# Optimization experiments

Measured on AMD Instinct MI355X. Metric: run time of the kernel, lower is better.

## Reference

```python
import jax, jax.numpy as jnp
import numpy as np

D_MODEL = 2048
HQ = 32          # query heads
HKV = 8          # kv heads
HD = D_MODEL // HQ   # head_dim = 64
G = HQ // HKV        # group size = 4
THETA = 10000.0


def _rope(x, pos):
    """x: (B, H, T, D), pos: (B, T) int. Rotates even/odd interleaved pairs."""
    D = x.shape[-1]
    inv_freq = THETA ** (-jnp.arange(0, D, 2, dtype=jnp.float32) / D)   # (D/2,)
    ang = pos[:, None, :, None].astype(jnp.float32) * inv_freq          # (B,1,T,D/2)
    cos, sin = jnp.cos(ang), jnp.sin(ang)
    x1, x2 = x[..., 0::2], x[..., 1::2]
    r1 = x1 * cos - x2 * sin
    r2 = x1 * sin + x2 * cos
    return jnp.stack([r1, r2], axis=-1).reshape(x.shape)


def setup_inputs() -> dict:
    key = jax.random.key(0)
    ks = jax.random.split(key, 5)
    B, T = 2, 2048
    s = lambda fan_in: 1.0 / np.sqrt(fan_in)
    return {
        "x": jax.random.normal(ks[0], (B, T, D_MODEL), jnp.float32),
        "token_positions": jnp.arange(T, dtype=jnp.int32),
        "WQ": jax.random.normal(ks[1], (HQ * HD, D_MODEL), jnp.float32) * s(D_MODEL),
        "WK": jax.random.normal(ks[2], (HKV * HD, D_MODEL), jnp.float32) * s(D_MODEL),
        "WV": jax.random.normal(ks[3], (HKV * HD, D_MODEL), jnp.float32) * s(D_MODEL),
        "WO": jax.random.normal(ks[4], (D_MODEL, HQ * HD), jnp.float32) * s(HQ * HD),
    }


def reference(x, token_positions, WQ, WK, WV, WO):
    B, T, _ = x.shape
    pos = token_positions if token_positions.ndim == 2 else jnp.broadcast_to(token_positions[None, :], (B, T))

    # Projections (Linear is y = x @ W.T, no bias)
    Q = (x @ WQ.T).reshape(B, T, HQ, HD).transpose(0, 2, 1, 3)    # (B,Hq,T,D)
    K = (x @ WK.T).reshape(B, T, HKV, HD).transpose(0, 2, 1, 3)   # (B,Hkv,T,D)
    V = (x @ WV.T).reshape(B, T, HKV, HD).transpose(0, 2, 1, 3)

    Q = _rope(Q, pos)
    K = _rope(K, pos)

    # GQA: group query heads per kv head instead of duplicating K/V
    Qg = Q.reshape(B, HKV, G, T, HD)
    scale = jnp.float32(1.0 / np.sqrt(HD))
    scores = jnp.einsum('bkgqd,bkld->bkgql', Qg, K) * scale       # (B,Hkv,G,T,T)

    causal = jnp.tril(jnp.ones((T, T), dtype=bool))
    scores = jnp.where(causal, scores, jnp.finfo(scores.dtype).min)
    A = jax.nn.softmax(scores, axis=-1)

    O = jnp.einsum('bkgql,bkld->bkgqd', A, V)                     # (B,Hkv,G,T,D)
    O = O.reshape(B, HQ, T, HD).transpose(0, 2, 1, 3).reshape(B, T, HQ * HD)
    return O @ WO.T
```

## Files before the change

kernel.cpp:

```cpp
#include <hip/hip_runtime.h>
#include <hip/hip_bf16.h>

#define B_   2
#define T_   2048
#define DM_  2048
#define HQ_  32
#define HKV_ 8
#define HD_  64

typedef __attribute__((ext_vector_type(8))) short bf16x8;
typedef __attribute__((ext_vector_type(4))) float f32x4;
typedef __fp16 f16x4 __attribute__((ext_vector_type(4)));
typedef __fp16 f16x2 __attribute__((ext_vector_type(2)));

__device__ __forceinline__ unsigned short f2bf(float f) {
    unsigned int u = __float_as_uint(f);
    u = (u + 0x7fffu + ((u >> 16) & 1u)) >> 16;
    return (unsigned short)u;
}

__device__ __forceinline__ void gload16(const unsigned short* g, unsigned short* l) {
    __builtin_amdgcn_global_load_lds(
        (const __attribute__((address_space(1))) unsigned int*)g,
        (__attribute__((address_space(3))) unsigned int*)l, 16, 0, 0);
}


__global__ __launch_bounds__(256) void convert_all(
    const float* __restrict__ x,  const float* __restrict__ WQ,
    const float* __restrict__ WK, const float* __restrict__ WV,
    const float* __restrict__ WO, unsigned short* __restrict__ ws)
{
    int i = blockIdx.x*256 + threadIdx.x;
    const float* src; unsigned short* dst; int rel;
    if (i < 2097152)      { src = x;  dst = ws;                 rel = i; }
    else if (i < 3145728) { src = WQ; dst = ws + 8388608;       rel = i - 2097152; }
    else if (i < 3407872) { src = WK; dst = ws + 8388608+4194304; rel = i - 3145728; }
    else if (i < 3670016) { src = WV; dst = ws + 8388608+5242880; rel = i - 3407872; }
    else                  { src = WO; dst = ws + 14680064;      rel = i - 3670016; }
    float4 v = *(const float4*)(src + (size_t)rel*4);
    uint2 pk;
    pk.x = (unsigned int)f2bf(v.x) | ((unsigned int)f2bf(v.y) << 16);
    pk.y = (unsigned int)f2bf(v.z) | ((unsigned int)f2bf(v.w) << 16);
    *(uint2*)(dst + (size_t)rel*4) = pk;
}

__global__ __launch_bounds__(256) void qkv_gemm_bf16(
    const unsigned short* __restrict__ Ab, const unsigned short* __restrict__ Wb,
    unsigned short* __restrict__ Qb, unsigned short* __restrict__ Kb,
    unsigned short* __restrict__ Vt)
{
    __shared__ unsigned short As[128*32];
    __shared__ unsigned short Bs[128*32];
    const int tid  = threadIdx.x;
    const int ln   = tid & 63;
    const int wv   = tid >> 6;
    const int wm   = (wv >> 1) * 64;
    const int wn   = (wv & 1) * 64;
    const int col  = ln & 15;
    const int quad = ln >> 4;
    const int m0   = blockIdx.y * 128;
    const int n0   = blockIdx.x * 128;

    const unsigned short* aG = Ab + (size_t)(m0 + (tid>>2))*DM_ + (tid&3)*8;
    const unsigned short* bG = Wb + (size_t)(n0 + (tid>>2))*DM_ + (tid&3)*8;
    unsigned short* aL0 = &As[wv*512];
    unsigned short* aL1 = &As[wv*512 + 2048];
    unsigned short* bL0 = &Bs[wv*512];
    unsigned short* bL1 = &Bs[wv*512 + 2048];

    f32x4 acc[4][4];
    #pragma unroll
    for (int i=0;i<4;++i)
        #pragma unroll
        for (int j=0;j<4;++j) { acc[i][j][0]=0.f; acc[i][j][1]=0.f; acc[i][j][2]=0.f; acc[i][j][3]=0.f; }

    for (int k0 = 0; k0 < DM_; k0 += 32) {
        __syncthreads();
        gload16(aG + k0,                  aL0);
        gload16(aG + (size_t)64*DM_ + k0, aL1);
        gload16(bG + k0,                  bL0);
        gload16(bG + (size_t)64*DM_ + k0, bL1);
        __syncthreads();
        bf16x8 af[4], bfr[4];
        #pragma unroll
        for (int i=0;i<4;++i) {
            af[i]  = *(const bf16x8*)&As[(wm + i*16 + col)*32 + quad*8];
            bfr[i] = *(const bf16x8*)&Bs[(wn + i*16 + col)*32 + quad*8];
        }
        #pragma unroll
        for (int i=0;i<4;++i)
            #pragma unroll
            for (int j=0;j<4;++j)
                acc[i][j] = __builtin_amdgcn_mfma_f32_16x16x32_bf16(af[i], bfr[j], acc[i][j], 0, 0, 0);
    }

    const int b  = m0 >> 11;
    const int tb = m0 & 2047;
    #pragma unroll
    for (int j=0;j<4;++j) {
        const int n = n0 + wn + j*16 + col;
        #pragma unroll
        for (int i=0;i<4;++i) {
            const int t = tb + wm + i*16 + quad*4;
            if (n < 2048) {
                #pragma unroll
                for (int r=0;r<4;++r)
                    Qb[(((size_t)(b*HQ_ + (n>>6)))*T_ + t + r)*HD_ + (n&63)] = f2bf(acc[i][j][r]);
            } else if (n < 2560) {
                #pragma unroll
                for (int r=0;r<4;++r)
                    Kb[(((size_t)(b*HKV_ + ((n-2048)>>6)))*T_ + t + r)*HD_ + (n&63)] = f2bf(acc[i][j][r]);
            } else {
                unsigned short* vp = Vt + (((size_t)(b*HKV_ + ((n-2560)>>6)))*HD_ + (n&63))*T_ + t;
                union { f16x2 h; unsigned int u; } c0, c1;
                c0.h = __builtin_amdgcn_cvt_pkrtz(acc[i][j][0], acc[i][j][1]);
                c1.h = __builtin_amdgcn_cvt_pkrtz(acc[i][j][2], acc[i][j][3]);
                *(unsigned int*)(vp)     = c0.u;
                *(unsigned int*)(vp + 2) = c1.u;
            }
        }
    }
}

__global__ __launch_bounds__(256) void rope_inplace(
    unsigned short* __restrict__ Qb, unsigned short* __restrict__ Kb,
    const int* __restrict__ pos)
{
    const int NQ = B_*HQ_*T_*(HD_/2);
    const int NK = B_*HKV_*T_*(HD_/2);
    int idx = blockIdx.x*256 + threadIdx.x;
    unsigned short* base; float scale;
    int rem;
    if (idx < NQ) { base = Qb; rem = idx; scale = 0.18033688011112042f; }
    else { rem = idx - NQ; if (rem >= NK) return; base = Kb; scale = 1.0f; }
    const int i  = rem & 31;
    const int t  = (rem >> 5) & (T_ - 1);
    const int bh = rem >> 16;
    size_t off = (((size_t)bh)*T_ + t)*HD_ + (i<<1);
    unsigned int pk = *(unsigned int*)(base + off);
    float x1 = __uint_as_float((pk & 0xffffu) << 16);
    float x2 = __uint_as_float(pk & 0xffff0000u);
    float p = (float)pos[t];
    float inv = exp2f(-13.287712379549449f * ((float)(i<<1)) * (1.0f/64.0f));
    float ang = p * inv;
    float sn, cs;
    sincosf(ang, &sn, &cs);
    float r1 = (x1*cs - x2*sn) * scale;
    float r2 = (x1*sn + x2*cs) * scale;
    unsigned int out = (unsigned int)f2bf(r1) | ((unsigned int)f2bf(r2) << 16);
    *(unsigned int*)(base + off) = out;
}

__global__ __launch_bounds__(256, 2) void attn_mfma(
    const unsigned short* __restrict__ Qb, const unsigned short* __restrict__ Kb,
    const unsigned short* __restrict__ Vh, unsigned short* __restrict__ Ob)
{
    __shared__ unsigned short Ks[64*64];
    __shared__ unsigned short Vs[64*64];

    const int tid  = threadIdx.x;
    const int lane = tid & 63;
    const int wave = tid >> 6;
    const int q16  = lane & 15;
    const int quad = lane >> 4;
    const int bxi  = blockIdx.x;
    const int bh   = blockIdx.y;
    const int b    = bh >> 5;
    const int h    = bh & 31;
    const int kvh  = h >> 2;
    const int qa   = bxi;
    const int qbt  = 31 - bxi;
    const int qgA  = qa *64 + wave*16 + q16;
    const int qgB  = qbt*64 + wave*16 + q16;

    const unsigned short* kbase = Kb + ((size_t)(b*HKV_ + kvh))*T_*HD_;
    const unsigned short* vbase = Vh + ((size_t)(b*HKV_ + kvh))*(size_t)HD_*T_;

    const bf16x8 qA0 = *(const bf16x8*)(Qb + ((size_t)bh*T_ + qgA)*HD_ + quad*8);
    const bf16x8 qA1 = *(const bf16x8*)(Qb + ((size_t)bh*T_ + qgA)*HD_ + 32 + quad*8);
    const bf16x8 qB0 = *(const bf16x8*)(Qb + ((size_t)bh*T_ + qgB)*HD_ + quad*8);
    const bf16x8 qB1 = *(const bf16x8*)(Qb + ((size_t)bh*T_ + qgB)*HD_ + 32 + quad*8);

    f32x4 oA[4], oB[4];
    #pragma unroll
    for (int i=0;i<4;++i) {
        oA[i][0]=0.f; oA[i][1]=0.f; oA[i][2]=0.f; oA[i][3]=0.f;
        oB[i][0]=0.f; oB[i][1]=0.f; oB[i][2]=0.f; oB[i][3]=0.f;
    }
    float lA = 0.f, lB = 0.f;

    const int sr = tid >> 3;
    const int sj = tid & 7;
    const int sc = (sj ^ (sr & 7)) * 8;
    uint4 kr0, kr1, vr0, vr1;

    const int rk7 = q16 & 7;
    const int ck0 = (quad ^ rk7) * 8;
    const int ck1 = ((quad + 4) ^ rk7) * 8;

    kr0 = *(const uint4*)(kbase + (size_t)sr*HD_ + sj*8);
    kr1 = *(const uint4*)(kbase + (size_t)(sr+32)*HD_ + sj*8);
    vr0 = *(const uint4*)(vbase + (size_t)sr*T_ + sj*8);
    vr1 = *(const uint4*)(vbase + (size_t)(sr+32)*T_ + sj*8);

    for (int kt = 0; kt <= qbt; ++kt) {
        const int k0 = kt * 64;
        __syncthreads();
        *(uint4*)&Ks[sr*64 + sc]      = kr0;
        *(uint4*)&Ks[(sr+32)*64 + sc] = kr1;
        *(uint4*)&Vs[sr*64 + sc]      = vr0;
        *(uint4*)&Vs[(sr+32)*64 + sc] = vr1;
        __syncthreads();
        if (kt < qbt) {
            const int kn = k0 + 64;
            kr0 = *(const uint4*)(kbase + (size_t)(kn+sr)*HD_ + sj*8);
            kr1 = *(const uint4*)(kbase + (size_t)(kn+sr+32)*HD_ + sj*8);
            vr0 = *(const uint4*)(vbase + (size_t)sr*T_ + kn + sj*8);
            vr1 = *(const uint4*)(vbase + (size_t)(sr+32)*T_ + kn + sj*8);
        }
        const bool doA = (kt <= qa);

        f32x4 sAq[4], sBq[4];
        #pragma unroll
        for (int t=0;t<4;++t) {
            sAq[t][0]=0.f; sAq[t][1]=0.f; sAq[t][2]=0.f; sAq[t][3]=0.f;
            sBq[t][0]=0.f; sBq[t][1]=0.f; sBq[t][2]=0.f; sBq[t][3]=0.f;
        }
        #pragma unroll
        for (int t = 0; t < 4; ++t) {
            const int rk = (t*16 + q16) * 64;
            bf16x8 a0 = *(const bf16x8*)&Ks[rk + ck0];
            bf16x8 a1 = *(const bf16x8*)&Ks[rk + ck1];
            sBq[t] = __builtin_amdgcn_mfma_f32_16x16x32_bf16(a0, qB0, sBq[t], 0, 0, 0);
            sBq[t] = __builtin_amdgcn_mfma_f32_16x16x32_bf16(a1, qB1, sBq[t], 0, 0, 0);
            if (doA) {
                sAq[t] = __builtin_amdgcn_mfma_f32_16x16x32_bf16(a0, qA0, sAq[t], 0, 0, 0);
                sAq[t] = __builtin_amdgcn_mfma_f32_16x16x32_bf16(a1, qA1, sAq[t], 0, 0, 0);
            }
        }
        if (kt == qbt) {
            #pragma unroll
            for (int t = 0; t < 4; ++t)
                #pragma unroll
                for (int r = 0; r < 4; ++r)
                    if (k0 + t*16 + quad*4 + r > qgB) sBq[t][r] = -1e30f;
        }
        if (doA && kt == qa) {
            #pragma unroll
            for (int t = 0; t < 4; ++t)
                #pragma unroll
                for (int r = 0; r < 4; ++r)
                    if (k0 + t*16 + quad*4 + r > qgA) sAq[t][r] = -1e30f;
        }

        f16x4 pfA[4], pfB[4];
        float psA = 0.f, psB = 0.f;
        #pragma unroll
        for (int t = 0; t < 4; ++t) {
            float b0 = exp2f(sBq[t][0]), b1 = exp2f(sBq[t][1]);
            float b2 = exp2f(sBq[t][2]), b3 = exp2f(sBq[t][3]);
            psB += (b0+b1) + (b2+b3);
            union { f16x2 h[2]; f16x4 v; } cb;
            cb.h[0] = __builtin_amdgcn_cvt_pkrtz(b0, b1);
            cb.h[1] = __builtin_amdgcn_cvt_pkrtz(b2, b3);
            pfB[t] = cb.v;
        }
        lB += psB;
        if (doA) {
            #pragma unroll
            for (int t = 0; t < 4; ++t) {
                float a0 = exp2f(sAq[t][0]), a1 = exp2f(sAq[t][1]);
                float a2 = exp2f(sAq[t][2]), a3 = exp2f(sAq[t][3]);
                psA += (a0+a1) + (a2+a3);
                union { f16x2 h[2]; f16x4 v; } ca;
                ca.h[0] = __builtin_amdgcn_cvt_pkrtz(a0, a1);
                ca.h[1] = __builtin_amdgcn_cvt_pkrtz(a2, a3);
                pfA[t] = ca.v;
            }
            lA += psA;
        }

        #pragma unroll
        for (int dt = 0; dt < 4; ++dt) {
            const int rv = (dt*16 + q16) * 64;
            #pragma unroll
            for (int t = 0; t < 4; ++t) {
                const int cv = ((2*t + (quad>>1)) ^ rk7) * 8 + (quad&1)*4;
                f16x4 va = *(const f16x4*)&Vs[rv + cv];
                oB[dt] = __builtin_amdgcn_mfma_f32_16x16x16f16(va, pfB[t], oB[dt], 0, 0, 0);
                if (doA)
                    oA[dt] = __builtin_amdgcn_mfma_f32_16x16x16f16(va, pfA[t], oA[dt], 0, 0, 0);
            }
        }
    }

    lA += __shfl_xor(lA, 16); lA += __shfl_xor(lA, 32);
    lB += __shfl_xor(lB, 16); lB += __shfl_xor(lB, 32);
    const float rlA = 1.0f / lA;
    const float rlB = 1.0f / lB;
    unsigned short* opA = Ob + ((size_t)(b*T_ + qgA))*(HQ_*HD_) + h*HD_;
    unsigned short* opB = Ob + ((size_t)(b*T_ + qgB))*(HQ_*HD_) + h*HD_;
    #pragma unroll
    for (int dt = 0; dt < 4; ++dt) {
        uint2 pa, pb;
        pa.x = (unsigned int)f2bf(oA[dt][0]*rlA) | ((unsigned int)f2bf(oA[dt][1]*rlA) << 16);
        pa.y = (unsigned int)f2bf(oA[dt][2]*rlA) | ((unsigned int)f2bf(oA[dt][3]*rlA) << 16);
        pb.x = (unsigned int)f2bf(oB[dt][0]*rlB) | ((unsigned int)f2bf(oB[dt][1]*rlB) << 16);
        pb.y = (unsigned int)f2bf(oB[dt][2]*rlB) | ((unsigned int)f2bf(oB[dt][3]*rlB) << 16);
        *(uint2*)(opA + dt*16 + quad*4) = pa;
        *(uint2*)(opB + dt*16 + quad*4) = pb;
    }
}

__global__ __launch_bounds__(256) void out_gemm_bf16(
    const unsigned short* __restrict__ Ab, const unsigned short* __restrict__ Wb,
    float* __restrict__ C)
{
    __shared__ unsigned short As[128*32];
    __shared__ unsigned short Bs[128*32];
    const int tid  = threadIdx.x;
    const int ln   = tid & 63;
    const int wv   = tid >> 6;
    const int wm   = (wv >> 1) * 64;
    const int wn   = (wv & 1) * 64;
    const int col  = ln & 15;
    const int quad = ln >> 4;
    const int m0   = blockIdx.y * 128;
    const int n0   = blockIdx.x * 128;

    const unsigned short* aG = Ab + (size_t)(m0 + (tid>>2))*DM_ + (tid&3)*8;
    const unsigned short* bG = Wb + (size_t)(n0 + (tid>>2))*DM_ + (tid&3)*8;
    unsigned short* aL0 = &As[wv*512];
    unsigned short* aL1 = &As[wv*512 + 2048];
    unsigned short* bL0 = &Bs[wv*512];
    unsigned short* bL1 = &Bs[wv*512 + 2048];

    f32x4 acc[4][4];
    #pragma unroll
    for (int i=0;i<4;++i)
        #pragma unroll
        for (int j=0;j<4;++j) { acc[i][j][0]=0.f; acc[i][j][1]=0.f; acc[i][j][2]=0.f; acc[i][j][3]=0.f; }

    for (int k0 = 0; k0 < DM_; k0 += 32) {
        __syncthreads();
        gload16(aG + k0,                  aL0);
        gload16(aG + (size_t)64*DM_ + k0, aL1);
        gload16(bG + k0,                  bL0);
        gload16(bG + (size_t)64*DM_ + k0, bL1);
        __syncthreads();
        bf16x8 af[4], bfr[4];
        #pragma unroll
        for (int i=0;i<4;++i) {
            af[i]  = *(const bf16x8*)&As[(wm + i*16 + col)*32 + quad*8];
            bfr[i] = *(const bf16x8*)&Bs[(wn + i*16 + col)*32 + quad*8];
        }
        #pragma unroll
        for (int i=0;i<4;++i)
            #pragma unroll
            for (int j=0;j<4;++j)
                acc[i][j] = __builtin_amdgcn_mfma_f32_16x16x32_bf16(af[i], bfr[j], acc[i][j], 0, 0, 0);
    }

    #pragma unroll
    for (int i=0;i<4;++i) {
        const int m = m0 + wm + i*16 + quad*4;
        #pragma unroll
        for (int j=0;j<4;++j) {
            const int n = n0 + wn + j*16 + col;
            #pragma unroll
            for (int r=0;r<4;++r)
                C[(size_t)(m + r)*DM_ + n] = acc[i][j][r];
        }
    }
}

extern "C" void kernel_launch(void* const* d_in, const int* in_sizes, int n_in,
                              void* d_out, int out_size, void* d_ws, size_t ws_size,
                              hipStream_t stream) {
    const float* x   = (const float*)d_in[0];
    const int*   pos = (const int*)  d_in[1];
    const float* WQ  = (const float*)d_in[2];
    const float* WK  = (const float*)d_in[3];
    const float* WV  = (const float*)d_in[4];
    const float* WO  = (const float*)d_in[5];
    float* out = (float*)d_out;

    unsigned short* xb  = (unsigned short*)d_ws;
    unsigned short* Wb  = xb  + (size_t)8388608;
    unsigned short* WOb = Wb  + (size_t)6291456;
    unsigned short* Qb  = WOb + (size_t)4194304;
    unsigned short* Kb  = Qb  + (size_t)8388608;
    unsigned short* Vt  = Kb  + (size_t)2097152;
    unsigned short* Ob  = Vt  + (size_t)2097152;

    convert_all<<<18432, 256, 0, stream>>>(x, WQ, WK, WV, WO, (unsigned short*)d_ws);

    dim3 g1(24, 32);
    qkv_gemm_bf16<<<g1, 256, 0, stream>>>(xb, Wb, Qb, Kb, Vt);

    const int pairs = B_*HQ_*T_*(HD_/2) + B_*HKV_*T_*(HD_/2);
    rope_inplace<<<(pairs + 255)/256, 256, 0, stream>>>(Qb, Kb, pos);

    dim3 g3(16, B_*HQ_);
    attn_mfma<<<g3, 256, 0, stream>>>(Qb, Kb, Vt, Ob);

    dim3 g4(16, 32);
    out_gemm_bf16<<<g4, 256, 0, stream>>>(Ob, WOb, out);
}
```

Measured before the change: 359.8 us.

## Double-buffer K/V tiles in LDS and split attention loop into paired/single phases

Replaces the single LDS K/V buffer with two buffers, so the next tile is written to LDS while the current one is consumed, leaving one barrier per iteration instead of two. The kv loop is split into a phase where both query tiles are active and a phase with only the far tile, which removes the per-iteration doA branches. Softmax exponentials are interleaved with the MFMA issue, and s_setprio raises wave priority around the compute. This doubles LDS use (32KB per block), which may affect occupancy at 2 blocks/CU, and makes the instruction schedule more complex.

After: 337.7 us. 6.1% less time.

```diff
diff --git a/kernel.cpp b/kernel.cpp
--- a/kernel.cpp
+++ b/kernel.cpp
@@ -156,8 +156,8 @@
     const unsigned short* __restrict__ Qb, const unsigned short* __restrict__ Kb,
     const unsigned short* __restrict__ Vh, unsigned short* __restrict__ Ob)
 {
-    __shared__ unsigned short Ks[64*64];
-    __shared__ unsigned short Vs[64*64];
+    __shared__ unsigned short Ks[2][64*64];
+    __shared__ unsigned short Vs[2][64*64];
 
     const int tid  = threadIdx.x;
     const int lane = tid & 63;
@@ -193,106 +193,161 @@
     const int sr = tid >> 3;
     const int sj = tid & 7;
     const int sc = (sj ^ (sr & 7)) * 8;
-    uint4 kr0, kr1, vr0, vr1;
 
     const int rk7 = q16 & 7;
     const int ck0 = (quad ^ rk7) * 8;
     const int ck1 = ((quad + 4) ^ rk7) * 8;
 
+    auto smrow = [&](const f32x4 s, float& ps) -> f16x4 {
+        float e0 = exp2f(s[0]), e1 = exp2f(s[1]);
+        float e2 = exp2f(s[2]), e3 = exp2f(s[3]);
+        ps += (e0+e1) + (e2+e3);
+        union { f16x2 h[2]; f16x4 v; } c;
+        c.h[0] = __builtin_amdgcn_cvt_pkrtz(e0, e1);
+        c.h[1] = __builtin_amdgcn_cvt_pkrtz(e2, e3);
+        return c.v;
+    };
+
+    uint4 kr0, kr1, vr0, vr1;
     kr0 = *(const uint4*)(kbase + (size_t)sr*HD_ + sj*8);
     kr1 = *(const uint4*)(kbase + (size_t)(sr+32)*HD_ + sj*8);
     vr0 = *(const uint4*)(vbase + (size_t)sr*T_ + sj*8);
     vr1 = *(const uint4*)(vbase + (size_t)(sr+32)*T_ + sj*8);
-
-    for (int kt = 0; kt <= qbt; ++kt) {
-        const int k0 = kt * 64;
-        __syncthreads();
-        *(uint4*)&Ks[sr*64 + sc]      = kr0;
-        *(uint4*)&Ks[(sr+32)*64 + sc] = kr1;
-        *(uint4*)&Vs[sr*64 + sc]      = vr0;
-        *(uint4*)&Vs[(sr+32)*64 + sc] = vr1;
-        __syncthreads();
-        if (kt < qbt) {
-            const int kn = k0 + 64;
+    *(uint4*)&Ks[0][sr*64 + sc]      = kr0;
+    *(uint4*)&Ks[0][(sr+32)*64 + sc] = kr1;
+    *(uint4*)&Vs[0][sr*64 + sc]      = vr0;
+    *(uint4*)&Vs[0][(sr+32)*64 + sc] = vr1;
+    kr0 = *(const uint4*)(kbase + (size_t)(64+sr)*HD_ + sj*8);
+    kr1 = *(const uint4*)(kbase + (size_t)(64+sr+32)*HD_ + sj*8);
+    vr0 = *(const uint4*)(vbase + (size_t)sr*T_ + 64 + sj*8);
+    vr1 = *(const uint4*)(vbase + (size_t)(sr+32)*T_ + 64 + sj*8);
+    __syncthreads();
+
+    int cur = 0;
+
+    for (int kt = 0; kt <= qa; ++kt) {
+        const unsigned short* KsC = Ks[cur];
+        const unsigned short* VsC = Vs[cur];
+        const int nxt = cur ^ 1;
+
+        f32x4 sB[4], sA[4];
+        #pragma unroll
+        for (int t=0;t<4;++t) {
+            sB[t][0]=0.f; sB[t][1]=0.f; sB[t][2]=0.f; sB[t][3]=0.f;
+            sA[t][0]=0.f; sA[t][1]=0.f; sA[t][2]=0.f; sA[t][3]=0.f;
+        }
+        f16x4 pfB[4];
+        float psB = 0.f, psA = 0.f;
+
+        __builtin_amdgcn_s_setprio(1);
+        #pragma unroll
+        for (int t = 0; t < 4; ++t) {
+            const int rk = (t*16 + q16) * 64;
+            bf16x8 a0 = *(const bf16x8*)&KsC[rk + ck0];
+            bf16x8 a1 = *(const bf16x8*)&KsC[rk + ck1];
+            sB[t] = __builtin_amdgcn_mfma_f32_16x16x32_bf16(a0, qB0, sB[t], 0, 0, 0);
+            sB[t] = __builtin_amdgcn_mfma_f32_16x16x32_bf16(a1, qB1, sB[t], 0, 0, 0);
+            sA[t] = __builtin_amdgcn_mfma_f32_16x16x32_bf16(a0, qA0, sA[t], 0, 0, 0);
+            sA[t] = __builtin_amdgcn_mfma_f32_16x16x32_bf16(a1, qA1, sA[t], 0, 0, 0);
+            if (t > 0) pfB[t-1] = smrow(sB[t-1], psB);
+        }
+        *(uint4*)&Ks[nxt][sr*64 + sc]      = kr0;
+        *(uint4*)&Ks[nxt][(sr+32)*64 + sc] = kr1;
+        *(uint4*)&Vs[nxt][sr*64 + sc]      = vr0;
+        *(uint4*)&Vs[nxt][(sr+32)*64 + sc] = vr1;
+        if (kt + 1 < qbt) {
+            const int kn = (kt+2)*64;
             kr0 = *(const uint4*)(kbase + (size_t)(kn+sr)*HD_ + sj*8);
             kr1 = *(const uint4*)(kbase + (size_t)(kn+sr+32)*HD_ + sj*8);
             vr0 = *(const uint4*)(vbase + (size_t)sr*T_ + kn + sj*8);
             vr1 = *(const uint4*)(vbase + (size_t)(sr+32)*T_ + kn + sj*8);
         }
-        const bool doA = (kt <= qa);
-
-        f32x4 sAq[4], sBq[4];
-        #pragma unroll
-        for (int t=0;t<4;++t) {
-            sAq[t][0]=0.f; sAq[t][1]=0.f; sAq[t][2]=0.f; sAq[t][3]=0.f;
-            sBq[t][0]=0.f; sBq[t][1]=0.f; sBq[t][2]=0.f; sBq[t][3]=0.f;
-        }
-        #pragma unroll
-        for (int t = 0; t < 4; ++t) {
-            const int rk = (t*16 + q16) * 64;
-            bf16x8 a0 = *(const bf16x8*)&Ks[rk + ck0];
-            bf16x8 a1 = *(const bf16x8*)&Ks[rk + ck1];
-            sBq[t] = __builtin_amdgcn_mfma_f32_16x16x32_bf16(a0, qB0, sBq[t], 0, 0, 0);
-            sBq[t] = __builtin_amdgcn_mfma_f32_16x16x32_bf16(a1, qB1, sBq[t], 0, 0, 0);
-            if (doA) {
-                sAq[t] = __builtin_amdgcn_mfma_f32_16x16x32_bf16(a0, qA0, sAq[t], 0, 0, 0);
-                sAq[t] = __builtin_amdgcn_mfma_f32_16x16x32_bf16(a1, qA1, sAq[t], 0, 0, 0);
-            }
-        }
-        if (kt == qbt) {
+        pfB[3] = smrow(sB[3], psB);
+        lB += psB;
+
+        if (kt == qa) {
             #pragma unroll
             for (int t = 0; t < 4; ++t)
                 #pragma unroll
                 for (int r = 0; r < 4; ++r)
-                    if (k0 + t*16 + quad*4 + r > qgB) sBq[t][r] = -1e30f;
-        }
-        if (doA && kt == qa) {
+                    if (kt*64 + t*16 + quad*4 + r > qgA) sA[t][r] = -1e30f;
+        }
+
+        #pragma unroll
+        for (int t = 0; t < 4; ++t) {
+            const int cv = ((2*t + (quad>>1)) ^ rk7) * 8 + (quad&1)*4;
+            f16x4 va[4];
+            #pragma unroll
+            for (int dt=0;dt<4;++dt)
+                va[dt] = *(const f16x4*)&VsC[(dt*16 + q16)*64 + cv];
+            #pragma unroll
+            for (int dt=0;dt<4;++dt)
+                oB[dt] = __builtin_amdgcn_mfma_f32_16x16x16f16(va[dt], pfB[t], oB[dt], 0, 0, 0);
+            f16x4 pfA = smrow(sA[t], psA);
+            #pragma unroll
+            for (int dt=0;dt<4;++dt)
+                oA[dt] = __builtin_amdgcn_mfma_f32_16x16x16f16(va[dt], pfA, oA[dt], 0, 0, 0);
+        }
+        lA += psA;
+        __builtin_amdgcn_s_setprio(0);
+        __syncthreads();
+        cur ^= 1;
+    }
+
+    for (int kt = qa+1; kt <= qbt; ++kt) {
+        const unsigned short* KsC = Ks[cur];
+        const unsigned short* VsC = Vs[cur];
+        const int nxt = cur ^ 1;
+
+        f32x4 sB[4];
+        #pragma unroll
+        for (int t=0;t<4;++t) { sB[t][0]=0.f; sB[t][1]=0.f; sB[t][2]=0.f; sB[t][3]=0.f; }
+
+        __builtin_amdgcn_s_setprio(1);
+        #pragma unroll
+        for (int t = 0; t < 4; ++t) {
+            const int rk = (t*16 + q16) * 64;
+            bf16x8 a0 = *(const bf16x8*)&KsC[rk + ck0];
+            bf16x8 a1 = *(const bf16x8*)&KsC[rk + ck1];
+            sB[t] = __builtin_amdgcn_mfma_f32_16x16x32_bf16(a0, qB0, sB[t], 0, 0, 0);
+            sB[t] = __builtin_amdgcn_mfma_f32_16x16x32_bf16(a1, qB1, sB[t], 0, 0, 0);
+        }
+        if (kt < qbt) {
+            *(uint4*)&Ks[nxt][sr*64 + sc]      = kr0;
+            *(uint4*)&Ks[nxt][(sr+32)*64 + sc] = kr1;
+            *(uint4*)&Vs[nxt][sr*64 + sc]      = vr0;
+            *(uint4*)&Vs[nxt][(sr+32)*64 + sc] = vr1;
+        }
+        if (kt + 1 < qbt) {
+            const int kn = (kt+2)*64;
+            kr0 = *(const uint4*)(kbase + (size_t)(kn+sr)*HD_ + sj*8);
+            kr1 = *(const uint4*)(kbase + (size_t)(kn+sr+32)*HD_ + sj*8);
+            vr0 = *(const uint4*)(vbase + (size_t)sr*T_ + kn + sj*8);
+            vr1 = *(const uint4*)(vbase + (size_t)(sr+32)*T_ + kn + sj*8);
+        }
+        if (kt == qbt) {
             #pragma unroll
             for (int t = 0; t < 4; ++t)
                 #pragma unroll
                 for (int r = 0; r < 4; ++r)
-                    if (k0 + t*16 + quad*4 + r > qgA) sAq[t][r] = -1e30f;
-        }
-
-        f16x4 pfA[4], pfB[4];
-        float psA = 0.f, psB = 0.f;
+                    if (kt*64 + t*16 + quad*4 + r > qgB) sB[t][r] = -1e30f;
+        }
+
+        float psB = 0.f;
         #pragma unroll
         for (int t = 0; t < 4; ++t) {
-            float b0 = exp2f(sBq[t][0]), b1 = exp2f(sBq[t][1]);
-            float b2 = exp2f(sBq[t][2]), b3 = exp2f(sBq[t][3]);
-            psB += (b0+b1) + (b2+b3);
-            union { f16x2 h[2]; f16x4 v; } cb;
-            cb.h[0] = __builtin_amdgcn_cvt_pkrtz(b0, b1);
-            cb.h[1] = __builtin_amdgcn_cvt_pkrtz(b2, b3);
-            pfB[t] = cb.v;
+            f16x4 pfB = smrow(sB[t], psB);
+            const int cv = ((2*t + (quad>>1)) ^ rk7) * 8 + (quad&1)*4;
+            #pragma unroll
+            for (int dt=0;dt<4;++dt) {
+                f16x4 va = *(const f16x4*)&VsC[(dt*16 + q16)*64 + cv];
+                oB[dt] = __builtin_amdgcn_mfma_f32_16x16x16f16(va, pfB, oB[dt], 0, 0, 0);
+            }
         }
         lB += psB;
-        if (doA) {
-            #pragma unroll
-            for (int t = 0; t < 4; ++t) {
-                float a0 = exp2f(sAq[t][0]), a1 = exp2f(sAq[t][1]);
-                float a2 = exp2f(sAq[t][2]), a3 = exp2f(sAq[t][3]);
-                psA += (a0+a1) + (a2+a3);
-                union { f16x2 h[2]; f16x4 v; } ca;
-                ca.h[0] = __builtin_amdgcn_cvt_pkrtz(a0, a1);
-                ca.h[1] = __builtin_amdgcn_cvt_pkrtz(a2, a3);
-                pfA[t] = ca.v;
-            }
-            lA += psA;
-        }
-
-        #pragma unroll
-        for (int dt = 0; dt < 4; ++dt) {
-            const int rv = (dt*16 + q16) * 64;
-            #pragma unroll
-            for (int t = 0; t < 4; ++t) {
-                const int cv = ((2*t + (quad>>1)) ^ rk7) * 8 + (quad&1)*4;
-                f16x4 va = *(const f16x4*)&Vs[rv + cv];
-                oB[dt] = __builtin_amdgcn_mfma_f32_16x16x16f16(va, pfB[t], oB[dt], 0, 0, 0);
-                if (doA)
-                    oA[dt] = __builtin_amdgcn_mfma_f32_16x16x16f16(va, pfA[t], oA[dt], 0, 0, 0);
-            }
-        }
+        __builtin_amdgcn_s_setprio(0);
+        __syncthreads();
+        cur ^= 1;
     }
 
     lA += __shfl_xor(lA, 16); lA += __shfl_xor(lA, 32);
```
